# Kernel tuning notes

Measured on AMD Instinct MI355X. Metric: run time of the kernel, lower is better.

## Reference

```python
import jax, jax.numpy as jnp
import numpy as np

B, N_PER, P_PER = 64, 64, 2016   # graphs, nodes/graph, pairs/graph (C(64,2))
IN_DIM, HID, OUT = 64, 128, 10
EDGE_P = 0.125


def _build_graph_structures():
    """Integer preprocessing replicating build_2sets_from_embeddings's
    combinatorics (pairs, iso_type source, triangle-based 2-set edges)."""
    rng = np.random.default_rng(0)
    n, b = N_PER, B
    A = rng.random((b, n, n)) < EDGE_P
    A = np.triu(A, 1)
    A = A | A.transpose(0, 2, 1)                      # symmetric, no self loops
    gs, us, vs = np.nonzero(A)                        # directed edges, both dirs
    edge_index = np.stack([gs * n + us, gs * n + vs]).astype(np.int64)
    batch = np.repeat(np.arange(b), n).astype(np.int64)
    iu, iv = np.triu_indices(n, 1)                    # local pair (u<v) lists
    pidx = np.full((n, n), -1, np.int64)
    pidx[iu, iv] = np.arange(P_PER)
    pidx[iv, iu] = np.arange(P_PER)                   # symmetric lookup = sorted()
    pair_u = (np.arange(b)[:, None] * n + iu[None, :]).ravel().astype(np.int64)
    pair_v = (np.arange(b)[:, None] * n + iv[None, :]).ravel().astype(np.int64)
    iso_type = A[:, iu, iv].astype(np.float32).ravel()[:, None]  # [B*P_PER,1]
    # 2-set edges: pair (u,v) -> sorted(v,w) and sorted(u,w) for every common
    # neighbor w of u and v (matches _build_2set_edges exactly)
    common = A[:, iu, :] & A[:, iv, :]                # (B, P_PER, n)
    g2, ps, ws = np.nonzero(common)
    u, v = iu[ps], iv[ps]
    d1 = pidx[v, ws]
    d2 = pidx[u, ws]
    src = np.concatenate([g2 * P_PER + ps, g2 * P_PER + ps])
    dst = np.concatenate([g2 * P_PER + d1, g2 * P_PER + d2])
    two_edges = np.stack([src, dst]).astype(np.int64)
    two_batch = np.repeat(np.arange(b), P_PER).astype(np.int64)
    return edge_index, batch, pair_u, pair_v, iso_type, two_edges, two_batch


def setup_inputs() -> dict:
    ei, batch, pu, pv, iso, te, tb = _build_graph_structures()
    key = jax.random.key(0)
    ks = jax.random.split(key, 16)
    w = lambda k, i, o: jax.random.normal(k, (i, o), jnp.float32) / np.float32(np.sqrt(i))
    two_in = 2 * HID + 1
    return {
        "x": jax.random.normal(ks[0], (B * N_PER, IN_DIM), jnp.float32),
        "g1_W1_0": w(ks[1], IN_DIM, HID), "g1_W2_0": w(ks[2], IN_DIM, HID),
        "g1_W1_1": w(ks[3], HID, HID),    "g1_W2_1": w(ks[4], HID, HID),
        "g1_W1_2": w(ks[5], HID, HID),    "g1_W2_2": w(ks[6], HID, HID),
        "k_W1_0": w(ks[7], two_in, HID),  "k_W2_0": w(ks[8], two_in, HID),
        "k_W1_1": w(ks[9], HID, HID),     "k_W2_1": w(ks[10], HID, HID),
        "c_W0": w(ks[11], 2 * HID, HID),  "c_b0": jnp.zeros((HID,), jnp.float32),
        "c_W1": w(ks[12], HID, OUT),      "c_b1": jnp.zeros((OUT,), jnp.float32),
        "iso_type": jnp.asarray(iso),
        "edge_index": jnp.asarray(ei), "batch": jnp.asarray(batch),
        "pair_u": jnp.asarray(pu), "pair_v": jnp.asarray(pv),
        "two_edges": jnp.asarray(te), "two_batch": jnp.asarray(tb),
    }


def _mp_layer(h, ei, W1, W2):
    # relu( h @ W1 + scatter_add_{dst}( h[src] @ W2 ) )  -- OneGNNLayer / KSetLayer
    msg = h[ei[0]] @ W2
    agg = jax.ops.segment_sum(msg, ei[1], num_segments=h.shape[0])
    return jax.nn.relu(h @ W1 + agg)


def reference(x, g1_W1_0, g1_W2_0, g1_W1_1, g1_W2_1, g1_W1_2, g1_W2_2,
              k_W1_0, k_W2_0, k_W1_1, k_W2_1,
              c_W0, c_b0, c_W1, c_b1,
              iso_type, edge_index, batch, pair_u, pair_v, two_edges, two_batch):
    h = _mp_layer(x, edge_index, g1_W1_0, g1_W2_0)
    h = _mp_layer(h, edge_index, g1_W1_1, g1_W2_1)
    h = _mp_layer(h, edge_index, g1_W1_2, g1_W2_2)
    graph_emb_1 = jax.ops.segment_sum(h, batch, num_segments=B)
    # 2-set features: [h_u, h_v, iso_type]  -> [P, 2H+1]
    two_x = jnp.concatenate([h[pair_u], h[pair_v], iso_type], axis=1)
    h2 = _mp_layer(two_x, two_edges, k_W1_0, k_W2_0)
    h2 = _mp_layer(h2, two_edges, k_W1_1, k_W2_1)
    graph_emb_2 = jax.ops.segment_sum(h2, two_batch, num_segments=B)
    combined = jnp.concatenate([graph_emb_1, graph_emb_2], axis=1)
    hc = jax.nn.relu(combined @ c_W0 + c_b0)   # Dropout(p=0.5) inactive in eval
    return hc @ c_W1 + c_b1
```

## Files before the change

### kernel.cpp

```cpp
#include <hip/hip_runtime.h>
#include <hip/hip_bf16.h>


typedef short s16x8 __attribute__((ext_vector_type(8)));
typedef float f32x4 __attribute__((ext_vector_type(4)));

__device__ __forceinline__ unsigned short f2bf(float f) {
  union { float f; unsigned u; } x; x.f = f;
  unsigned r = (x.u + 0x7fffu + ((x.u >> 16) & 1u)) >> 16;
  return (unsigned short)r;
}
__device__ __forceinline__ float bf2f(unsigned short h) {
  union { unsigned u; float f; } x; x.u = ((unsigned)h) << 16;
  return x.f;
}
__device__ __forceinline__ float4 ldbf4(const unsigned short* p) {
  ushort4 q = *(const ushort4*)p;
  return make_float4(bf2f(q.x), bf2f(q.y), bf2f(q.z), bf2f(q.w));
}
__device__ __forceinline__ void stbf4(unsigned short* p, float4 v) {
  ushort4 q;
  q.x = f2bf(v.x); q.y = f2bf(v.y); q.z = f2bf(v.z); q.w = f2bf(v.w);
  *(ushort4*)p = q;
}
__device__ __forceinline__ float4 ld4(const float* p) { return *(const float4*)p; }

template<int KCS, int ASTR>
__device__ __forceinline__ void mfma_dual_lds(
    const unsigned short* A, const unsigned short* Wfrag,
    f32x4 (&accA)[8], f32x4 (&accB)[8])
{
  const int lane = threadIdx.x & 63;
  const int wv = threadIdx.x >> 6;
  const int row = wv * 16 + (lane & 15);
  const int k0 = (lane >> 4) << 3;
  const unsigned short* ap = A + row * ASTR + k0;
  const unsigned short* wp = Wfrag + (size_t)lane * 8;
#pragma unroll
  for (int i = 0; i < 8; ++i) { accA[i] = (f32x4)0.f; accB[i] = (f32x4)0.f; }
#pragma unroll
  for (int kc = 0; kc < KCS; ++kc) {
    s16x8 af = *(const s16x8*)(ap + kc * 32);
#pragma unroll
    for (int nt = 0; nt < 8; ++nt) {
      s16x8 b0 = *(const s16x8*)(wp + ((size_t)((nt)*KCS + kc) << 9));
      s16x8 b1 = *(const s16x8*)(wp + ((size_t)((8 + nt) * KCS + kc) << 9));
      accA[nt] = __builtin_amdgcn_mfma_f32_16x16x32_bf16(af, b0, accA[nt], 0, 0, 0);
      accB[nt] = __builtin_amdgcn_mfma_f32_16x16x32_bf16(af, b1, accB[nt], 0, 0, 0);
    }
  }
}

__device__ __forceinline__ void epi_lds(const f32x4 (&accA)[8], const f32x4 (&accB)[8],
    unsigned short (*preS)[136], unsigned short (*msgS)[136])
{
  const int lane = threadIdx.x & 63;
  const int wv = threadIdx.x >> 6;
  const int col = lane & 15;
  const int r0 = wv * 16 + ((lane >> 4) << 2);
  __syncthreads();
#pragma unroll
  for (int nt = 0; nt < 8; ++nt)
#pragma unroll
    for (int r = 0; r < 4; ++r) {
      preS[r0 + r][nt * 16 + col] = f2bf(accA[nt][r]);
      msgS[r0 + r][nt * 16 + col] = f2bf(accB[nt][r]);
    }
  __syncthreads();
}

__device__ __forceinline__ void epi_global(const f32x4 (&accA)[8], const f32x4 (&accB)[8],
    unsigned short (*sOut)[136], unsigned short* Ca, unsigned short* Cb, long tile)
{
  const int tid = threadIdx.x;
  const int lane = tid & 63;
  const int wv = tid >> 6;
  const int col = lane & 15;
  const int r0 = wv * 16 + ((lane >> 4) << 2);
  const long rowBase = tile * 64;
#pragma unroll
  for (int sel = 0; sel < 2; ++sel) {
    __syncthreads();
#pragma unroll
    for (int nt = 0; nt < 8; ++nt) {
#pragma unroll
      for (int r = 0; r < 4; ++r)
        sOut[r0 + r][nt * 16 + col] = f2bf(sel ? accB[nt][r] : accA[nt][r]);
    }
    __syncthreads();
    unsigned short* C = sel ? Cb : Ca;
#pragma unroll
    for (int i = 0; i < 4; ++i) {
      int fi = tid + i * 256;
      int row = fi >> 4;
      int c8 = fi & 15;
      *(uint4*)(C + (rowBase + row) * 128 + c8 * 8) = *(uint4*)&sOut[row][c8 * 8];
    }
  }
}

struct NArgs {
  const float* x;
  const int* ei;
  const int* gstart;
  const unsigned short *Wf0, *Wf1, *Wf2, *Wf3, *Wf4;
  unsigned short *HU1, *HV1, *HU2, *HV2;
  float* ge1;
  int E1;
};

__global__ __launch_bounds__(256) void node_stage(NArgs a)
{
  __shared__ __align__(16) unsigned short hS[64][136];
  __shared__ __align__(16) unsigned short preS[64][136];
  __shared__ __align__(16) unsigned short msgS[64][136];
  __shared__ int ldeg[64], lcur[64], loff[65];
  __shared__ unsigned short ledge[1024];
  __shared__ float sge[128];

  const int b = blockIdx.x;
  const int t = threadIdx.x;
  const int base = b * 64;

  const int es = a.gstart[b], ee = a.gstart[b + 1];
  if (t < 64) ldeg[t] = 0;
  if (t < 128) sge[t] = 0.f;
  __syncthreads();
  for (int i = es + t; i < ee; i += 256)
    atomicAdd(&ldeg[a.ei[a.E1 + i] - base], 1);
  __syncthreads();
  if (t < 64) {
    int v = ldeg[t], s = v;
#pragma unroll
    for (int d = 1; d < 64; d <<= 1) {
      int o = __shfl_up(s, d, 64);
      if (t >= d) s += o;
    }
    loff[t] = s - v;
    lcur[t] = s - v;
    if (t == 63) loff[64] = s;
  }
  unsigned short* xs = &preS[0][0];
  for (int i = t; i < 64 * 64; i += 256) {
    int r = i >> 6, c = i & 63;
    xs[r * 72 + c] = f2bf(a.x[(size_t)(base + r) * 64 + c]);
  }
  __syncthreads();
  for (int i = es + t; i < ee; i += 256) {
    int s = a.ei[i] - base, d = a.ei[a.E1 + i] - base;
    int pos = atomicAdd(&lcur[d], 1);
    ledge[pos] = (unsigned short)s;
  }
  __syncthreads();

  f32x4 accA[8], accB[8];
  const int grp = t >> 5, f = (t & 31) * 4;

  mfma_dual_lds<2, 72>(xs, a.Wf0, accA, accB);
  epi_lds(accA, accB, preS, msgS);
  for (int r = grp; r < 64; r += 8) {
    float4 acc = ldbf4(&preS[r][f]);
    int j1 = loff[r + 1];
    for (int j = loff[r]; j < j1; ++j) {
      float4 m = ldbf4(&msgS[ledge[j]][f]);
      acc.x += m.x; acc.y += m.y; acc.z += m.z; acc.w += m.w;
    }
    stbf4(&hS[r][f], make_float4(fmaxf(acc.x, 0.f), fmaxf(acc.y, 0.f),
                                 fmaxf(acc.z, 0.f), fmaxf(acc.w, 0.f)));
  }
  __syncthreads();

  mfma_dual_lds<4, 136>(&hS[0][0], a.Wf1, accA, accB);
  epi_lds(accA, accB, preS, msgS);
  for (int r = grp; r < 64; r += 8) {
    float4 acc = ldbf4(&preS[r][f]);
    int j1 = loff[r + 1];
    for (int j = loff[r]; j < j1; ++j) {
      float4 m = ldbf4(&msgS[ledge[j]][f]);
      acc.x += m.x; acc.y += m.y; acc.z += m.z; acc.w += m.w;
    }
    stbf4(&hS[r][f], make_float4(fmaxf(acc.x, 0.f), fmaxf(acc.y, 0.f),
                                 fmaxf(acc.z, 0.f), fmaxf(acc.w, 0.f)));
  }
  __syncthreads();

  mfma_dual_lds<4, 136>(&hS[0][0], a.Wf2, accA, accB);
  epi_lds(accA, accB, preS, msgS);
  {
    float4 g = make_float4(0.f, 0.f, 0.f, 0.f);
    for (int r = grp; r < 64; r += 8) {
      float4 acc = ldbf4(&preS[r][f]);
      int j1 = loff[r + 1];
      for (int j = loff[r]; j < j1; ++j) {
        float4 m = ldbf4(&msgS[ledge[j]][f]);
        acc.x += m.x; acc.y += m.y; acc.z += m.z; acc.w += m.w;
      }
      float4 o = make_float4(fmaxf(acc.x, 0.f), fmaxf(acc.y, 0.f),
                             fmaxf(acc.z, 0.f), fmaxf(acc.w, 0.f));
      stbf4(&hS[r][f], o);
      g.x += o.x; g.y += o.y; g.z += o.z; g.w += o.w;
    }
    atomicAdd(&sge[f + 0], g.x);
    atomicAdd(&sge[f + 1], g.y);
    atomicAdd(&sge[f + 2], g.z);
    atomicAdd(&sge[f + 3], g.w);
  }
  __syncthreads();
  if (t < 128) a.ge1[b * 128 + t] = sge[t];

  mfma_dual_lds<4, 136>(&hS[0][0], a.Wf3, accA, accB);
  epi_global(accA, accB, preS, a.HU1, a.HU2, b);
  mfma_dual_lds<4, 136>(&hS[0][0], a.Wf4, accA, accB);
  epi_global(accA, accB, preS, a.HV1, a.HV2, b);
}

struct PrepArgs {
  const float* wa[6];
  const float* wb[6];
  unsigned short* Wf[6];
  float* ge2;
  const int* te; int E2;
  int* degP;
  const int* ei; int E1;
  int* gstart;
  int nCnt;
};

__global__ void prep(PrepArgs p)
{
  int bb = blockIdx.x, t = threadIdx.x;
  if (bb < 88) {
    int gid = bb * 256 + t;
    if (gid < 22528) {
      int pi, local, kcs, kclog;
      if (gid < 2048) { pi = 0; local = gid; kcs = 2; kclog = 1; }
      else { int r = gid - 2048; pi = 1 + (r >> 12); local = r & 4095; kcs = 4; kclog = 2; }
      int lane = local & 63;
      int t1 = local >> 6;
      int kc = t1 & (kcs - 1);
      int t2 = t1 >> kclog;
      int nt = t2 & 7;
      int wsel = t2 >> 3;
      const float* W = wsel ? p.wb[pi] : p.wa[pi];
      int k0 = kc * 32 + ((lane >> 4) << 3);
      int n = nt * 16 + (lane & 15);
      unsigned short tmp[8];
#pragma unroll
      for (int j = 0; j < 8; ++j) tmp[j] = f2bf(W[(size_t)(k0 + j) * 128 + n]);
      *(uint4*)(p.Wf[pi] + (size_t)local * 8) = *(uint4*)tmp;
    }
  } else if (bb < 120) {
    int i = (bb - 88) * 256 + t;
    if (i < 8192) p.ge2[i] = 0.f;
  } else if (bb < 120 + p.nCnt) {
    int e = (bb - 120) * 256 + t;
    if (e < p.E2) atomicAdd(&p.degP[p.te[p.E2 + e]], 1);
  } else {
    int e = (bb - 120 - p.nCnt) * 256 + t;
    if (e <= p.E1) {
      int ge = (e < p.E1) ? (p.ei[e] >> 6) : 64;
      int gp = (e > 0) ? (p.ei[e - 1] >> 6) : -1;
      for (int g = gp + 1; g <= ge; ++g) p.gstart[g] = e;
    }
  }
}

__global__ __launch_bounds__(256) void scan_reduce(const int* __restrict__ deg,
                                                   int* __restrict__ bsum, int n)
{
  __shared__ int s[256];
  int b = blockIdx.x, t = threadIdx.x;
  int base = b * 1024;
  int v = 0;
#pragma unroll
  for (int i = 0; i < 4; ++i) {
    int idx = base + t + i * 256;
    if (idx < n) v += deg[idx];
  }
  s[t] = v;
  __syncthreads();
  for (int d = 128; d > 0; d >>= 1) {
    if (t < d) s[t] += s[t + d];
    __syncthreads();
  }
  if (t == 0) bsum[b] = s[0];
}

__global__ __launch_bounds__(1024) void scan_partials(int* __restrict__ bsum, int nb)
{
  __shared__ int s[1024];
  int t = threadIdx.x;
  s[t] = (t < nb) ? bsum[t] : 0;
  __syncthreads();
  for (int d = 1; d < 1024; d <<= 1) {
    int v = (t >= d) ? s[t - d] : 0;
    __syncthreads();
    s[t] += v;
    __syncthreads();
  }
  if (t < nb) bsum[t] = (t == 0) ? 0 : s[t - 1];
  if (t == 1023) bsum[nb] = s[1023];
}

__global__ __launch_bounds__(256) void scan_final(const int* __restrict__ deg,
                                                  const int* __restrict__ bsum,
                                                  int* __restrict__ off,
                                                  int* __restrict__ cur, int n, int nb)
{
  __shared__ int s[256];
  int b = blockIdx.x, t = threadIdx.x;
  int base = b * 1024 + t * 4;
  int v0 = 0, v1 = 0, v2 = 0, v3 = 0;
  if (base + 0 < n) v0 = deg[base + 0];
  if (base + 1 < n) v1 = deg[base + 1];
  if (base + 2 < n) v2 = deg[base + 2];
  if (base + 3 < n) v3 = deg[base + 3];
  s[t] = v0 + v1 + v2 + v3;
  __syncthreads();
  for (int d = 1; d < 256; d <<= 1) {
    int v = (t >= d) ? s[t - d] : 0;
    __syncthreads();
    s[t] += v;
    __syncthreads();
  }
  int run = bsum[b] + ((t == 0) ? 0 : s[t - 1]);
  if (base + 0 < n) { off[base + 0] = run; cur[base + 0] = run; run += v0; }
  if (base + 1 < n) { off[base + 1] = run; cur[base + 1] = run; run += v1; }
  if (base + 2 < n) { off[base + 2] = run; cur[base + 2] = run; run += v2; }
  if (base + 3 < n) { off[base + 3] = run; cur[base + 3] = run; run += v3; }
  if (b == 0 && t == 0) off[n] = bsum[nb];
}

__global__ void csr_fill_pair(const int* __restrict__ te, int E2,
                              const int* __restrict__ pu, const int* __restrict__ pv,
                              const float* __restrict__ iso,
                              int* __restrict__ curP, int4* __restrict__ recP)
{
  int e = blockIdx.x * 256 + threadIdx.x;
  if (e >= E2) return;
  int s = te[e], d = te[E2 + e];
  int pos = atomicAdd(&curP[d], 1);
  recP[pos] = make_int4(pu[s], pv[s], __float_as_int(iso[s]), s);
}

__global__ __launch_bounds__(256) void gemm_dual_mfma4(
    const unsigned short* __restrict__ A, const unsigned short* __restrict__ Wfrag,
    unsigned short* __restrict__ Ca, unsigned short* __restrict__ Cb)
{
  __shared__ __align__(16) unsigned short sA[64][136];
  const int tid = threadIdx.x;
  const int lane = tid & 63;
  const int wv = tid >> 6;
  const long rowBase = (long)blockIdx.x * 64;

  f32x4 accA[8], accB[8];
#pragma unroll
  for (int i = 0; i < 8; ++i) { accA[i] = (f32x4)0.f; accB[i] = (f32x4)0.f; }

  const unsigned short* aptr =
      A + (size_t)(rowBase + wv * 16 + (lane & 15)) * 128 + ((lane >> 4) << 3);
  const unsigned short* wptr = Wfrag + (size_t)lane * 8;

#pragma unroll
  for (int kc = 0; kc < 4; ++kc) {
    s16x8 af = *(const s16x8*)(aptr + kc * 32);
#pragma unroll
    for (int nt = 0; nt < 8; ++nt) {
      s16x8 b0 = *(const s16x8*)(wptr + ((size_t)((nt)*4 + kc) << 9));
      s16x8 b1 = *(const s16x8*)(wptr + ((size_t)((8 + nt) * 4 + kc) << 9));
      accA[nt] = __builtin_amdgcn_mfma_f32_16x16x32_bf16(af, b0, accA[nt], 0, 0, 0);
      accB[nt] = __builtin_amdgcn_mfma_f32_16x16x32_bf16(af, b1, accB[nt], 0, 0, 0);
    }
  }
  epi_global(accA, accB, sA, Ca, Cb, blockIdx.x);
}

__global__ __launch_bounds__(256) void gather_two0_bf(
    const unsigned short* __restrict__ HU1, const unsigned short* __restrict__ HV1,
    const unsigned short* __restrict__ HU2, const unsigned short* __restrict__ HV2,
    const float* __restrict__ iso,
    const float* __restrict__ w1iso, const float* __restrict__ w2iso,
    const int* __restrict__ pu, const int* __restrict__ pv,
    const int* __restrict__ off, const int4* __restrict__ rec,
    unsigned short* __restrict__ out, int P)
{
  int p = blockIdx.x * 8 + (threadIdx.x >> 5);
  if (p >= P) return;
  int f = (threadIdx.x & 31) * 4;
  float4 wi1 = ld4(w1iso + f);
  float4 wi2 = ld4(w2iso + f);
  int u0 = pu[p], v0 = pv[p];
  float is0 = iso[p];
  float4 a = ldbf4(HU1 + (size_t)u0 * 128 + f);
  float4 b = ldbf4(HV1 + (size_t)v0 * 128 + f);
  float4 acc;
  acc.x = a.x + b.x + is0 * wi1.x;
  acc.y = a.y + b.y + is0 * wi1.y;
  acc.z = a.z + b.z + is0 * wi1.z;
  acc.w = a.w + b.w + is0 * wi1.w;
  int j = off[p], e1 = off[p + 1];
  for (; j + 1 < e1; j += 2) {
    int4 r0 = rec[j], r1 = rec[j + 1];
    float4 mu0 = ldbf4(HU2 + (size_t)r0.x * 128 + f);
    float4 mv0 = ldbf4(HV2 + (size_t)r0.y * 128 + f);
    float4 mu1 = ldbf4(HU2 + (size_t)r1.x * 128 + f);
    float4 mv1 = ldbf4(HV2 + (size_t)r1.y * 128 + f);
    float i0 = __int_as_float(r0.z), i1 = __int_as_float(r1.z);
    acc.x += mu0.x + mv0.x + i0 * wi2.x + mu1.x + mv1.x + i1 * wi2.x;
    acc.y += mu0.y + mv0.y + i0 * wi2.y + mu1.y + mv1.y + i1 * wi2.y;
    acc.z += mu0.z + mv0.z + i0 * wi2.z + mu1.z + mv1.z + i1 * wi2.z;
    acc.w += mu0.w + mv0.w + i0 * wi2.w + mu1.w + mv1.w + i1 * wi2.w;
  }
  if (j < e1) {
    int4 r0 = rec[j];
    float4 mu0 = ldbf4(HU2 + (size_t)r0.x * 128 + f);
    float4 mv0 = ldbf4(HV2 + (size_t)r0.y * 128 + f);
    float i0 = __int_as_float(r0.z);
    acc.x += mu0.x + mv0.x + i0 * wi2.x;
    acc.y += mu0.y + mv0.y + i0 * wi2.y;
    acc.z += mu0.z + mv0.z + i0 * wi2.z;
    acc.w += mu0.w + mv0.w + i0 * wi2.w;
  }
  stbf4(out + (size_t)p * 128 + f,
        make_float4(fmaxf(acc.x, 0.f), fmaxf(acc.y, 0.f),
                    fmaxf(acc.z, 0.f), fmaxf(acc.w, 0.f)));
}

__global__ __launch_bounds__(256) void gather_rec_segsum(
    const unsigned short* __restrict__ pre, const unsigned short* __restrict__ msg,
    const int* __restrict__ off, const int4* __restrict__ rec,
    float* __restrict__ ge2, int ppg)
{
  __shared__ float sF[128];
  int t = threadIdx.x;
  if (t < 128) sF[t] = 0.f;
  __syncthreads();
  int g = blockIdx.x >> 4;
  int sub = blockIdx.x & 15;
  int r0 = g * ppg + sub * 126;
  int grp = t >> 5;
  int f = (t & 31) * 4;
  float4 gacc = make_float4(0.f, 0.f, 0.f, 0.f);
  for (int rr = grp; rr < 126; rr += 8) {
    int r = r0 + rr;
    float4 acc = ldbf4(pre + (size_t)r * 128 + f);
    int j = off[r], e1 = off[r + 1];
    for (; j + 1 < e1; j += 2) {
      int4 q0 = rec[j], q1 = rec[j + 1];
      float4 m0 = ldbf4(msg + (size_t)q0.w * 128 + f);
      float4 m1 = ldbf4(msg + (size_t)q1.w * 128 + f);
      acc.x += m0.x + m1.x; acc.y += m0.y + m1.y;
      acc.z += m0.z + m1.z; acc.w += m0.w + m1.w;
    }
    if (j < e1) {
      int4 q0 = rec[j];
      float4 m0 = ldbf4(msg + (size_t)q0.w * 128 + f);
      acc.x += m0.x; acc.y += m0.y; acc.z += m0.z; acc.w += m0.w;
    }
    gacc.x += fmaxf(acc.x, 0.f); gacc.y += fmaxf(acc.y, 0.f);
    gacc.z += fmaxf(acc.z, 0.f); gacc.w += fmaxf(acc.w, 0.f);
  }
  atomicAdd(&sF[f + 0], gacc.x);
  atomicAdd(&sF[f + 1], gacc.y);
  atomicAdd(&sF[f + 2], gacc.z);
  atomicAdd(&sF[f + 3], gacc.w);
  __syncthreads();
  if (t < 128) atomicAdd(&ge2[g * 128 + t], sF[t]);
}

__global__ void classifier(const float* __restrict__ ge1, const float* __restrict__ ge2,
                           const float* __restrict__ W0, const float* __restrict__ b0,
                           const float* __restrict__ W1, const float* __restrict__ b1,
                           float* __restrict__ out)
{
  __shared__ float comb[256];
  __shared__ float hc[128];
  int g = blockIdx.x, t = threadIdx.x;
  comb[t]       = ge1[g * 128 + t];
  comb[t + 128] = ge2[g * 128 + t];
  __syncthreads();
  float s = b0[t];
  for (int k = 0; k < 256; ++k) s += comb[k] * W0[k * 128 + t];
  hc[t] = fmaxf(s, 0.f);
  __syncthreads();
  if (t < 10) {
    float s2 = b1[t];
    for (int k = 0; k < 128; ++k) s2 += hc[k] * W1[k * 10 + t];
    out[g * 10 + t] = s2;
  }
}

extern "C" void kernel_launch(void* const* d_in, const int* in_sizes, int n_in,
                              void* d_out, int out_size, void* d_ws, size_t ws_size,
                              hipStream_t stream)
{
  (void)n_in; (void)out_size; (void)ws_size;
  const float* x       = (const float*)d_in[0];
  const float* g1_W1_0 = (const float*)d_in[1];
  const float* g1_W2_0 = (const float*)d_in[2];
  const float* g1_W1_1 = (const float*)d_in[3];
  const float* g1_W2_1 = (const float*)d_in[4];
  const float* g1_W1_2 = (const float*)d_in[5];
  const float* g1_W2_2 = (const float*)d_in[6];
  const float* k_W1_0  = (const float*)d_in[7];
  const float* k_W2_0  = (const float*)d_in[8];
  const float* k_W1_1  = (const float*)d_in[9];
  const float* k_W2_1  = (const float*)d_in[10];
  const float* c_W0    = (const float*)d_in[11];
  const float* c_b0    = (const float*)d_in[12];
  const float* c_W1    = (const float*)d_in[13];
  const float* c_b1    = (const float*)d_in[14];
  const float* iso     = (const float*)d_in[15];
  const int*   ei      = (const int*)d_in[16];
  const int*   pu      = (const int*)d_in[18];
  const int*   pv      = (const int*)d_in[19];
  const int*   te      = (const int*)d_in[20];

  const int N  = in_sizes[0] / 64;
  const int E1 = in_sizes[16] / 2;
  const int P  = in_sizes[18];
  const int E2 = in_sizes[20] / 2;
  const int B  = 64;
  const int ppg = P / B;

  const size_t NH = (size_t)N * 128;
  const size_t PH = (size_t)P * 128;

  float* ge1 = (float*)d_ws;
  float* ge2 = ge1 + 8192;
  unsigned short* HU1 = (unsigned short*)(ge2 + 8192);
  unsigned short* HV1 = HU1 + NH;
  unsigned short* HU2 = HV1 + NH;
  unsigned short* HV2 = HU2 + NH;
  unsigned short* H2   = HV2 + NH;
  unsigned short* PRE2 = H2 + PH;
  unsigned short* MSG2 = PRE2 + PH;
  unsigned short* Wf0  = MSG2 + PH;
  unsigned short* Wf1  = Wf0 + 16384;
  unsigned short* Wf2  = Wf1 + 32768;
  unsigned short* Wf3  = Wf2 + 32768;
  unsigned short* Wf4  = Wf3 + 32768;
  unsigned short* Wf5  = Wf4 + 32768;

  size_t ipOff = ((size_t)((char*)(Wf5 + 32768) - (char*)d_ws) + 15) & ~(size_t)15;
  int4* recP   = (int4*)((char*)d_ws + ipOff);
  int* degP    = (int*)(recP + E2);
  int* offP    = degP + P;
  int* curP    = offP + P + 1;
  int* bsumP   = curP + P;
  int* gstartN = bsumP + 128;

  const int nbP  = (P + 1023) / 1024;
  const int nCnt = (E2 + 255) / 256;
  const int nBnd = (E1 + 256) / 256;

  hipMemsetAsync(degP, 0, (size_t)P * 4, stream);

  PrepArgs pa;
  pa.wa[0] = g1_W1_0;           pa.wb[0] = g1_W2_0;
  pa.wa[1] = g1_W1_1;           pa.wb[1] = g1_W2_1;
  pa.wa[2] = g1_W1_2;           pa.wb[2] = g1_W2_2;
  pa.wa[3] = k_W1_0;            pa.wb[3] = k_W2_0;
  pa.wa[4] = k_W1_0 + 128*128;  pa.wb[4] = k_W2_0 + 128*128;
  pa.wa[5] = k_W1_1;            pa.wb[5] = k_W2_1;
  pa.Wf[0] = Wf0; pa.Wf[1] = Wf1; pa.Wf[2] = Wf2;
  pa.Wf[3] = Wf3; pa.Wf[4] = Wf4; pa.Wf[5] = Wf5;
  pa.ge2 = ge2; pa.te = te; pa.E2 = E2; pa.degP = degP;
  pa.ei = ei; pa.E1 = E1; pa.gstart = gstartN; pa.nCnt = nCnt;
  prep<<<120 + nCnt + nBnd, 256, 0, stream>>>(pa);

  scan_reduce<<<nbP, 256, 0, stream>>>(degP, bsumP, P);
  scan_partials<<<1, 1024, 0, stream>>>(bsumP, nbP);
  scan_final<<<nbP, 256, 0, stream>>>(degP, bsumP, offP, curP, P, nbP);
  csr_fill_pair<<<nCnt, 256, 0, stream>>>(te, E2, pu, pv, iso, curP, recP);

  NArgs na;
  na.x = x; na.ei = ei; na.gstart = gstartN; na.E1 = E1;
  na.Wf0 = Wf0; na.Wf1 = Wf1; na.Wf2 = Wf2; na.Wf3 = Wf3; na.Wf4 = Wf4;
  na.HU1 = HU1; na.HU2 = HU2; na.HV1 = HV1; na.HV2 = HV2;
  na.ge1 = ge1;
  node_stage<<<B, 256, 0, stream>>>(na);

  gather_two0_bf<<<(P + 7) / 8, 256, 0, stream>>>(HU1, HV1, HU2, HV2, iso,
                                                  k_W1_0 + 256 * 128, k_W2_0 + 256 * 128,
                                                  pu, pv, offP, recP, H2, P);

  gemm_dual_mfma4<<<P / 64, 256, 0, stream>>>(H2, Wf5, PRE2, MSG2);

  gather_rec_segsum<<<B * 16, 256, 0, stream>>>(PRE2, MSG2, offP, recP, ge2, ppg);

  classifier<<<B, 128, 0, stream>>>(ge1, ge2, c_W0, c_b0, c_W1, c_b1, (float*)d_out);
}
```

Baseline: 318.6 us.

## Fuse pair layer-1 aggregation, dual GEMM and graph segment-sum into one kernel

Reorders the second 2-set layer to aggregate neighbor features first and then multiply by W2 (by linearity), fused with the h@W1 product in a single MFMA pass. The ReLU and per-graph sum are done in the same kernel, so the PRE2/MSG2 intermediates and one launch go away. Edge source indices for each tile are staged in LDS. The aggregated sum is rounded to bf16 before the GEMM, which adds slight precision change, and gathers now read from H2 rows.

After: 301.1 us. 1.06x faster.

```diff
diff --git a/kernel.cpp b/kernel.cpp
--- a/kernel.cpp
+++ b/kernel.cpp
@@ -341,38 +341,6 @@
   int s = te[e], d = te[E2 + e];
   int pos = atomicAdd(&curP[d], 1);
   recP[pos] = make_int4(pu[s], pv[s], __float_as_int(iso[s]), s);
-}
-
-__global__ __launch_bounds__(256) void gemm_dual_mfma4(
-    const unsigned short* __restrict__ A, const unsigned short* __restrict__ Wfrag,
-    unsigned short* __restrict__ Ca, unsigned short* __restrict__ Cb)
-{
-  __shared__ __align__(16) unsigned short sA[64][136];
-  const int tid = threadIdx.x;
-  const int lane = tid & 63;
-  const int wv = tid >> 6;
-  const long rowBase = (long)blockIdx.x * 64;
-
-  f32x4 accA[8], accB[8];
-#pragma unroll
-  for (int i = 0; i < 8; ++i) { accA[i] = (f32x4)0.f; accB[i] = (f32x4)0.f; }
-
-  const unsigned short* aptr =
-      A + (size_t)(rowBase + wv * 16 + (lane & 15)) * 128 + ((lane >> 4) << 3);
-  const unsigned short* wptr = Wfrag + (size_t)lane * 8;
-
-#pragma unroll
-  for (int kc = 0; kc < 4; ++kc) {
-    s16x8 af = *(const s16x8*)(aptr + kc * 32);
-#pragma unroll
-    for (int nt = 0; nt < 8; ++nt) {
-      s16x8 b0 = *(const s16x8*)(wptr + ((size_t)((nt)*4 + kc) << 9));
-      s16x8 b1 = *(const s16x8*)(wptr + ((size_t)((8 + nt) * 4 + kc) << 9));
-      accA[nt] = __builtin_amdgcn_mfma_f32_16x16x32_bf16(af, b0, accA[nt], 0, 0, 0);
-      accB[nt] = __builtin_amdgcn_mfma_f32_16x16x32_bf16(af, b1, accB[nt], 0, 0, 0);
-    }
-  }
-  epi_global(accA, accB, sA, Ca, Cb, blockIdx.x);
 }
 
 __global__ __launch_bounds__(256) void gather_two0_bf(
@@ -426,46 +394,107 @@
                     fmaxf(acc.z, 0.f), fmaxf(acc.w, 0.f)));
 }
 
-__global__ __launch_bounds__(256) void gather_rec_segsum(
-    const unsigned short* __restrict__ pre, const unsigned short* __restrict__ msg,
+__global__ __launch_bounds__(256) void pair_l1_fused(
+    const unsigned short* __restrict__ H2,
+    const unsigned short* __restrict__ Wfrag,
     const int* __restrict__ off, const int4* __restrict__ rec,
     float* __restrict__ ge2, int ppg)
 {
-  __shared__ float sF[128];
-  int t = threadIdx.x;
-  if (t < 128) sF[t] = 0.f;
-  __syncthreads();
-  int g = blockIdx.x >> 4;
-  int sub = blockIdx.x & 15;
-  int r0 = g * ppg + sub * 126;
-  int grp = t >> 5;
-  int f = (t & 31) * 4;
-  float4 gacc = make_float4(0.f, 0.f, 0.f, 0.f);
-  for (int rr = grp; rr < 126; rr += 8) {
-    int r = r0 + rr;
-    float4 acc = ldbf4(pre + (size_t)r * 128 + f);
-    int j = off[r], e1 = off[r + 1];
-    for (; j + 1 < e1; j += 2) {
-      int4 q0 = rec[j], q1 = rec[j + 1];
-      float4 m0 = ldbf4(msg + (size_t)q0.w * 128 + f);
-      float4 m1 = ldbf4(msg + (size_t)q1.w * 128 + f);
-      acc.x += m0.x + m1.x; acc.y += m0.y + m1.y;
-      acc.z += m0.z + m1.z; acc.w += m0.w + m1.w;
-    }
-    if (j < e1) {
-      int4 q0 = rec[j];
-      float4 m0 = ldbf4(msg + (size_t)q0.w * 128 + f);
-      acc.x += m0.x; acc.y += m0.y; acc.z += m0.z; acc.w += m0.w;
-    }
-    gacc.x += fmaxf(acc.x, 0.f); gacc.y += fmaxf(acc.y, 0.f);
-    gacc.z += fmaxf(acc.z, 0.f); gacc.w += fmaxf(acc.w, 0.f);
-  }
-  atomicAdd(&sF[f + 0], gacc.x);
-  atomicAdd(&sF[f + 1], gacc.y);
-  atomicAdd(&sF[f + 2], gacc.z);
-  atomicAdd(&sF[f + 3], gacc.w);
-  __syncthreads();
-  if (t < 128) atomicAdd(&ge2[g * 128 + t], sF[t]);
+  __shared__ __align__(16) unsigned short hS[64][136];
+  __shared__ __align__(16) unsigned short aggS[64][136];
+  __shared__ int offS[65];
+  __shared__ int recwS[768];
+  __shared__ float sge[2][128];
+
+  const int tid = threadIdx.x;
+  int tile = (int)blockIdx.x;
+  const int nT = (int)gridDim.x;
+  if ((nT & 7) == 0)
+    tile = (tile & 7) * (nT >> 3) + (tile >> 3);
+  const int r0 = tile * 64;
+
+  if (tid < 65) offS[tid] = off[r0 + tid];
+  if (tid < 128) { sge[0][tid] = 0.f; sge[1][tid] = 0.f; }
+  __syncthreads();
+
+  const int e0 = offS[0];
+  const int ecnt = offS[64] - e0;
+  const bool useS = (ecnt <= 768);
+  if (useS)
+    for (int j = tid; j < ecnt; j += 256) recwS[j] = rec[e0 + j].w;
+
+  {
+    const unsigned short* src = H2 + (size_t)r0 * 128;
+#pragma unroll
+    for (int i = 0; i < 4; ++i) {
+      int fi = tid + i * 256;
+      int row = fi >> 4, c8 = fi & 15;
+      *(uint4*)&hS[row][c8 * 8] = *(const uint4*)(src + row * 128 + c8 * 8);
+    }
+  }
+  __syncthreads();
+
+  {
+    const int grp = tid >> 5, f = (tid & 31) * 4;
+    for (int i = grp; i < 64; i += 8) {
+      float4 acc = make_float4(0.f, 0.f, 0.f, 0.f);
+      int j = offS[i], e1 = offS[i + 1];
+      for (; j + 1 < e1; j += 2) {
+        int s0 = useS ? recwS[j - e0] : rec[j].w;
+        int s1 = useS ? recwS[j + 1 - e0] : rec[j + 1].w;
+        float4 m0 = ldbf4(H2 + (size_t)s0 * 128 + f);
+        float4 m1 = ldbf4(H2 + (size_t)s1 * 128 + f);
+        acc.x += m0.x + m1.x; acc.y += m0.y + m1.y;
+        acc.z += m0.z + m1.z; acc.w += m0.w + m1.w;
+      }
+      if (j < e1) {
+        int s0 = useS ? recwS[j - e0] : rec[j].w;
+        float4 m0 = ldbf4(H2 + (size_t)s0 * 128 + f);
+        acc.x += m0.x; acc.y += m0.y; acc.z += m0.z; acc.w += m0.w;
+      }
+      stbf4(&aggS[i][f], acc);
+    }
+  }
+  __syncthreads();
+
+  const int lane = tid & 63;
+  const int wv = tid >> 6;
+  const int arow = wv * 16 + (lane & 15);
+  const int k0 = (lane >> 4) << 3;
+  const unsigned short* hp = &hS[0][0] + arow * 136 + k0;
+  const unsigned short* gp = &aggS[0][0] + arow * 136 + k0;
+  const unsigned short* wp = Wfrag + (size_t)lane * 8;
+  f32x4 acc[8];
+#pragma unroll
+  for (int nt = 0; nt < 8; ++nt) acc[nt] = (f32x4)0.f;
+  __builtin_amdgcn_s_setprio(1);
+#pragma unroll
+  for (int kc = 0; kc < 4; ++kc) {
+    s16x8 ah = *(const s16x8*)(hp + kc * 32);
+    s16x8 ag = *(const s16x8*)(gp + kc * 32);
+#pragma unroll
+    for (int nt = 0; nt < 8; ++nt) {
+      s16x8 b0 = *(const s16x8*)(wp + ((size_t)(nt * 4 + kc) << 9));
+      s16x8 b1 = *(const s16x8*)(wp + ((size_t)((8 + nt) * 4 + kc) << 9));
+      acc[nt] = __builtin_amdgcn_mfma_f32_16x16x32_bf16(ah, b0, acc[nt], 0, 0, 0);
+      acc[nt] = __builtin_amdgcn_mfma_f32_16x16x32_bf16(ag, b1, acc[nt], 0, 0, 0);
+    }
+  }
+  __builtin_amdgcn_s_setprio(0);
+
+  const int half = wv >> 1;
+  const int col0 = lane & 15;
+#pragma unroll
+  for (int nt = 0; nt < 8; ++nt) {
+    float s = fmaxf(acc[nt][0], 0.f) + fmaxf(acc[nt][1], 0.f)
+            + fmaxf(acc[nt][2], 0.f) + fmaxf(acc[nt][3], 0.f);
+    atomicAdd(&sge[half][nt * 16 + col0], s);
+  }
+  __syncthreads();
+  const int gLo = r0 / ppg;
+  const int gHi = (r0 + 32) / ppg;
+  if (tid < 128) atomicAdd(&ge2[gLo * 128 + tid], sge[0][tid]);
+  else           atomicAdd(&ge2[gHi * 128 + (tid - 128)], sge[1][tid - 128]);
 }
 
 __global__ void classifier(const float* __restrict__ ge1, const float* __restrict__ ge2,
@@ -533,9 +562,7 @@
   unsigned short* HU2 = HV1 + NH;
   unsigned short* HV2 = HU2 + NH;
   unsigned short* H2   = HV2 + NH;
-  unsigned short* PRE2 = H2 + PH;
-  unsigned short* MSG2 = PRE2 + PH;
-  unsigned short* Wf0  = MSG2 + PH;
+  unsigned short* Wf0  = H2 + PH;
   unsigned short* Wf1  = Wf0 + 16384;
   unsigned short* Wf2  = Wf1 + 32768;
   unsigned short* Wf3  = Wf2 + 32768;
@@ -585,9 +612,7 @@
                                                   k_W1_0 + 256 * 128, k_W2_0 + 256 * 128,
                                                   pu, pv, offP, recP, H2, P);
 
-  gemm_dual_mfma4<<<P / 64, 256, 0, stream>>>(H2, Wf5, PRE2, MSG2);
-
-  gather_rec_segsum<<<B * 16, 256, 0, stream>>>(PRE2, MSG2, offP, recP, ge2, ppg);
+  pair_l1_fused<<<P / 64, 256, 0, stream>>>(H2, Wf5, offP, recP, ge2, ppg);
 
   classifier<<<B, 128, 0, stream>>>(ge1, ge2, c_W0, c_b0, c_W1, c_b1, (float*)d_out);
 }
```
